# Optimization experiments

Measured on AMD Instinct MI355X. Metric: run time of the kernel, lower is better.

## Reference

```python
import math
import jax, jax.numpy as jnp
import numpy as np

NBINS = 10
MAX_ANGLE = math.pi
KERNEL = 8
POOL_PAD = 1
POOL_STRIDE = 1


def setup_inputs() -> dict:
    key = jax.random.key(0)
    x = jax.random.normal(key, (32, 1, 512, 512), dtype=jnp.float32)
    # Sobel buffer: mat stacked with its transpose -> [2, 1, 3, 3]
    mat = jnp.array([[1.0, 0.0, -1.0], [2.0, 0.0, -2.0], [1.0, 0.0, -1.0]], dtype=jnp.float32)
    weight = jnp.stack([mat, mat.T])[:, None, :, :]
    return {"x": x, "weight": weight}


def reference(x, weight):
    # Sobel gradients: conv2d, stride 1, padding 1 (cross-correlation, same as torch)
    gxy = jax.lax.conv_general_dilated(
        x, weight, window_strides=(1, 1),
        padding=[(1, 1), (1, 1)],
        dimension_numbers=("NCHW", "OIHW", "NCHW"))  # [N,2,H,W]

    norm = jnp.sqrt(gxy[:, 0] ** 2 + gxy[:, 1] ** 2)[:, None]        # [N,1,H,W]
    phase = jnp.arctan2(gxy[:, 0], gxy[:, 1])                        # [N,H,W]
    phase_int = (phase / MAX_ANGLE * NBINS)[:, None]                 # [N,1,H,W]

    # torch `%` is remainder (sign of divisor) == jnp.mod
    b = jnp.floor(phase_int) % NBINS
    t = jnp.ceil(phase_int) % NBINS
    f = phase_int % NBINS
    t_v = norm * (1.0 - (t - f))
    b_v = norm * (1.0 - (f - b))

    idx_b = jnp.floor(phase_int).astype(jnp.int32) % NBINS           # [N,1,H,W]
    idx_t = jnp.ceil(phase_int).astype(jnp.int32) % NBINS

    # scatter into nbins channels: out starts at zero, scatter_ (set) then
    # scatter_add_ -> equivalent to sum of the two one-hot contributions
    bins = jnp.arange(NBINS, dtype=jnp.int32)[None, :, None, None]   # [1,nbins,1,1]
    out = jnp.where(bins == idx_b, b_v, 0.0) + jnp.where(bins == idx_t, t_v, 0.0)  # [N,nbins,H,W]

    # AvgPool2d(kernel=8, stride=1, padding=1, count_include_pad=True)
    summed = jax.lax.reduce_window(
        out, 0.0, jax.lax.add,
        window_dimensions=(1, 1, KERNEL, KERNEL),
        window_strides=(1, 1, POOL_STRIDE, POOL_STRIDE),
        padding=[(0, 0), (0, 0), (POOL_PAD, POOL_PAD), (POOL_PAD, POOL_PAD)])
    return summed / float(KERNEL * KERNEL)
```

## Files before the change

kernel.cpp:

```cpp
#include <hip/hip_runtime.h>
#include <math.h>

#define NB 10
#define H 512
#define W 512
#define HW (H * W)
#define OH 507
#define OW 507
#define TW 32
#define TH 16
#define HC 39
#define HCP 40
#define HR 23
#define IC 41
#define IR 25
#define BD 512
#define BSTRIDE (HR * HCP)
#define HISTF (NB * BSTRIDE)
#define GX 16
#define GY 32
#define NIMG 32
#define NWG (GX * GY * NIMG)

__device__ __forceinline__ float f32mod10(float a) {
    float r = fmodf(a, 10.0f);
    if (r < 0.0f) r = __fadd_rn(r, 10.0f);
    return r;
}

__global__ __launch_bounds__(BD, 8)
void hog_fused(const float* __restrict__ x, float* __restrict__ out) {
    __shared__ __align__(16) float hist[HISTF];
    __shared__ __align__(16) float xin[IR * IC];

    const int orig = blockIdx.x;
    const int swz  = (orig & 7) * (NWG / 8) + (orig >> 3);
    const int tx   = swz & (GX - 1);
    const int ty   = (swz >> 4) & (GY - 1);
    const int n    = swz >> 9;

    const int tid = threadIdx.x;
    const int ox0 = tx * TW;
    const int oy0 = ty * TH;
    const float* __restrict__ xp = x + (size_t)n * HW;

    const int i1 = tid, i2 = tid + BD;
    int r1 = i1 / IC, c1 = i1 - r1 * IC;
    int r2 = i2 / IC, c2 = i2 - r2 * IC;
    int gy1 = oy0 - 2 + r1, gx1 = ox0 - 2 + c1;
    int gy2 = oy0 - 2 + r2, gx2 = ox0 - 2 + c2;
    const bool v1 = (unsigned)gy1 < H && (unsigned)gx1 < W;
    const bool v2 = (unsigned)gy2 < H && (unsigned)gx2 < W;
    float pv1 = v1 ? xp[gy1 * W + gx1] : 0.0f;
    float pv2 = v2 ? xp[gy2 * W + gx2] : 0.0f;
    float pv3 = 0.0f;
    if (tid == 0 && (unsigned)(oy0 + 22) < H && (unsigned)(ox0 + 38) < W)
        pv3 = xp[(oy0 + 22) * W + (ox0 + 38)];

    {
        float4* h4 = (float4*)hist;
        for (int i = tid; i < HISTF / 4; i += BD)
            h4[i] = make_float4(0.f, 0.f, 0.f, 0.f);
    }
    xin[i1] = pv1;
    xin[i2] = pv2;
    if (tid == 0) xin[1024] = pv3;
    __syncthreads();

    for (int p = tid; p < HR * HC; p += BD) {
        int hr = p / HC, hc = p - (p / HC) * HC;
        int hy = oy0 - 1 + hr, hx = ox0 - 1 + hc;
        if ((unsigned)hy >= H || (unsigned)hx >= W) continue;
        const float* xr = &xin[hr * IC + hc];
        float a00 = xr[0],      a01 = xr[1],          a02 = xr[2];
        float a10 = xr[IC],                           a12 = xr[IC + 2];
        float a20 = xr[2 * IC], a21 = xr[2 * IC + 1], a22 = xr[2 * IC + 2];

        float gxv = __fadd_rn(a00, -a02);
        gxv = __fadd_rn(gxv, __fmul_rn(2.0f, a10));
        gxv = __fadd_rn(gxv, -__fmul_rn(2.0f, a12));
        gxv = __fadd_rn(gxv, a20);
        gxv = __fadd_rn(gxv, -a22);
        float gyv = __fadd_rn(a00, __fmul_rn(2.0f, a01));
        gyv = __fadd_rn(gyv, a02);
        gyv = __fadd_rn(gyv, -a20);
        gyv = __fadd_rn(gyv, -__fmul_rn(2.0f, a21));
        gyv = __fadd_rn(gyv, -a22);

        float ay_ = fabsf(gxv), ax_ = fabsf(gyv);
        float hi = fmaxf(ax_, ay_), lo = fminf(ax_, ay_);
        if (hi == 0.0f) continue;
        float nrm = __builtin_amdgcn_sqrtf(
            __fadd_rn(__fmul_rn(gxv, gxv), __fmul_rn(gyv, gyv)));

        bool exact = (hi < 1e-30f) || (hi > 1e30f);
        float pint = 0.0f;
        if (!exact) {
            float t  = lo * __builtin_amdgcn_rcpf(hi);
            bool red = t > 0.41421356f;
            float u  = red ? (t - 1.0f) * __builtin_amdgcn_rcpf(t + 1.0f) : t;
            float z  = u * u;
            float pl = ((8.05374449538e-2f * z - 1.38776856032e-1f) * z
                        + 1.99777106478e-1f) * z - 3.33329491539e-1f;
            float a  = fmaf(u * z, pl, u);
            if (red) a += 0.78539816339744831f;
            if (ay_ > ax_) a = 1.57079632679489662f - a;
            if (gyv < 0.0f) a = 3.14159265358979324f - a;
            float ph = (gxv < 0.0f) ? -a : a;
            pint = ph * 3.18309886183790672f;
            if (fabsf(pint - rintf(pint)) < 1e-4f) exact = true;
        }

        float b_v, t_v;
        int ib, it;
        if (exact) {
            float phf = (float)atan2((double)gxv, (double)gyv);
            float pe  = __fmul_rn(__fdiv_rn(phf, (float)3.14159265358979323846), 10.0f);
            float bfv = floorf(pe), tfv = ceilf(pe);
            float fm = f32mod10(pe), bm = f32mod10(bfv), tm = f32mod10(tfv);
            t_v = __fmul_rn(nrm, __fsub_rn(1.0f, __fsub_rn(tm, fm)));
            b_v = __fmul_rn(nrm, __fsub_rn(1.0f, __fsub_rn(fm, bm)));
            ib = (((int)bfv % NB) + NB) % NB;
            it = (((int)tfv % NB) + NB) % NB;
        } else {
            float bfv  = floorf(pint);
            float frac = pint - bfv;
            float fm   = (pint < 0.0f) ? pint + 10.0f : pint;
            b_v = nrm * (1.0f - frac);
            int bi = (int)bfv;
            ib = (bi < 0) ? bi + 10 : bi;
            if (ib == 9) { it = 0;      t_v = nrm * (1.0f + fm); }
            else         { it = ib + 1; t_v = nrm * frac; }
        }
        int cell = hr * HCP + hc;
        if (ib == it) {
            hist[ib * BSTRIDE + cell] = __fadd_rn(b_v, t_v);
        } else {
            hist[ib * BSTRIDE + cell] = b_v;
            hist[it * BSTRIDE + cell] = t_v;
        }
    }
    __syncthreads();

    for (int q = tid; q < NB * (HCP / 4); q += BD) {
        int b = q / 10, c4 = q - (q / 10) * 10;
        float4* col = (float4*)&hist[b * BSTRIDE + c4 * 4];
        float4 s = make_float4(0.f, 0.f, 0.f, 0.f);
        #pragma unroll
        for (int hr = 0; hr < 8; ++hr) {
            float4 v = col[hr * 10];
            s.x += v.x; s.y += v.y; s.z += v.z; s.w += v.w;
        }
        float4 s0 = s;
        #pragma unroll 4
        for (int i = 1; i < TH; ++i) {
            float4 a = col[(i + 7) * 10];
            float4 d = col[(i - 1) * 10];
            s.x += a.x - d.x; s.y += a.y - d.y;
            s.z += a.z - d.z; s.w += a.w - d.w;
            col[(i - 1) * 10] = s;
        }
        col[22 * 10] = s0;
    }
    __syncthreads();

    float* __restrict__ outn = out + (size_t)n * (NB * OH * OW);
    const float4* h4 = (const float4*)hist;
    for (int u = tid; u < NB * TH * 4; u += BD) {
        int b = u >> 6, i = (u >> 2) & 15, g8 = u & 3;
        int rowf4 = b * (BSTRIDE / 4) + (i == 0 ? 22 : i - 1) * 10 + 2 * g8;
        float4 A = h4[rowf4], B = h4[rowf4 + 1], C = h4[rowf4 + 2], D = h4[rowf4 + 3];
        float o0 = ((A.x + A.y) + (A.z + A.w)) + ((B.x + B.y) + (B.z + B.w));
        float o1 = o0 - A.x + C.x;
        float o2 = o1 - A.y + C.y;
        float o3 = o2 - A.z + C.z;
        float o4 = o3 - A.w + C.w;
        float o5 = o4 - B.x + D.x;
        float o6 = o5 - B.y + D.y;
        float o7 = o6 - B.z + D.z;
        int oy = oy0 + i;
        if (oy < OH) {
            int oxg = ox0 + 8 * g8;
            float* po = outn + (size_t)(b * OH + oy) * OW + oxg;
            if (oxg + 7 < OW) {
                po[0] = o0 * (1.0f / 64.0f); po[1] = o1 * (1.0f / 64.0f);
                po[2] = o2 * (1.0f / 64.0f); po[3] = o3 * (1.0f / 64.0f);
                po[4] = o4 * (1.0f / 64.0f); po[5] = o5 * (1.0f / 64.0f);
                po[6] = o6 * (1.0f / 64.0f); po[7] = o7 * (1.0f / 64.0f);
            } else {
                float ov[8] = {o0, o1, o2, o3, o4, o5, o6, o7};
                #pragma unroll
                for (int j = 0; j < 8; ++j)
                    if (oxg + j < OW) po[j] = ov[j] * (1.0f / 64.0f);
            }
        }
    }
}

extern "C" void kernel_launch(void* const* d_in, const int* in_sizes, int n_in,
                              void* d_out, int out_size, void* d_ws, size_t ws_size,
                              hipStream_t stream) {
    const float* x = (const float*)d_in[0];
    float* out = (float*)d_out;
    hog_fused<<<dim3(NWG), dim3(BD), 0, stream>>>(x, out);
}
```

Measured before the change: 151.6 us.

## Make each workgroup loop over four column tiles with double-buffered histograms

Each workgroup now handles four horizontally adjacent 32x16 tiles in a loop instead of one. The next tile's input is prefetched into registers, the previous tile's output is written from one histogram buffer, and the current tile is scattered into the other buffer. This overlaps global loads and stores with compute and amortizes launch and setup costs across tiles. In exchange it doubles the histogram shared memory, lowers the occupancy hint from 8 to 4, and launches four times fewer workgroups, so there is less parallelism to hide latency.

New measurement: 158.0 us. 1.04x slower.

```diff
diff --git a/kernel.cpp b/kernel.cpp
--- a/kernel.cpp
+++ b/kernel.cpp
@@ -15,12 +15,14 @@
 #define IC 41
 #define IR 25
 #define BD 512
+#define KT 4
 #define BSTRIDE (HR * HCP)
 #define HISTF (NB * BSTRIDE)
-#define GX 16
+#define XINF (IR * IC)
+#define GXS 4
 #define GY 32
 #define NIMG 32
-#define NWG (GX * GY * NIMG)
+#define NWG (GXS * GY * NIMG)
 
 __device__ __forceinline__ float f32mod10(float a) {
     float r = fmodf(a, 10.0f);
@@ -28,172 +30,206 @@
     return r;
 }
 
-__global__ __launch_bounds__(BD, 8)
-void hog_fused(const float* __restrict__ x, float* __restrict__ out) {
-    __shared__ __align__(16) float hist[HISTF];
-    __shared__ __align__(16) float xin[IR * IC];
+__global__ __launch_bounds__(BD, 4)
+void hog_pipe(const float* __restrict__ x, float* __restrict__ out) {
+    __shared__ __align__(16) float hist[2][HISTF];
+    __shared__ __align__(16) float xin[XINF];
 
     const int orig = blockIdx.x;
     const int swz  = (orig & 7) * (NWG / 8) + (orig >> 3);
-    const int tx   = swz & (GX - 1);
-    const int ty   = (swz >> 4) & (GY - 1);
-    const int n    = swz >> 9;
+    const int bxs  = swz & (GXS - 1);
+    const int ty   = (swz >> 2) & (GY - 1);
+    const int n    = swz >> 7;
 
     const int tid = threadIdx.x;
-    const int ox0 = tx * TW;
+    const int oxb = bxs * (KT * TW);
     const int oy0 = ty * TH;
     const float* __restrict__ xp = x + (size_t)n * HW;
-
-    const int i1 = tid, i2 = tid + BD;
-    int r1 = i1 / IC, c1 = i1 - r1 * IC;
-    int r2 = i2 / IC, c2 = i2 - r2 * IC;
-    int gy1 = oy0 - 2 + r1, gx1 = ox0 - 2 + c1;
-    int gy2 = oy0 - 2 + r2, gx2 = ox0 - 2 + c2;
-    const bool v1 = (unsigned)gy1 < H && (unsigned)gx1 < W;
-    const bool v2 = (unsigned)gy2 < H && (unsigned)gx2 < W;
-    float pv1 = v1 ? xp[gy1 * W + gx1] : 0.0f;
-    float pv2 = v2 ? xp[gy2 * W + gx2] : 0.0f;
-    float pv3 = 0.0f;
-    if (tid == 0 && (unsigned)(oy0 + 22) < H && (unsigned)(ox0 + 38) < W)
-        pv3 = xp[(oy0 + 22) * W + (ox0 + 38)];
-
+    float* __restrict__ outn = out + (size_t)n * (NB * OH * OW);
+
+    const int i2 = tid + BD;
+    const int r1 = tid / IC, c1 = tid - r1 * IC;
+    const int r2 = i2 / IC,  c2 = i2 - r2 * IC;
+    const int gy1 = oy0 - 2 + r1, gy2 = oy0 - 2 + r2;
+    const int sp2 = tid + BD;
+    const int hr1 = tid / HC, hc1 = tid - hr1 * HC;
+    const int hr2 = sp2 / HC, hc2 = sp2 - hr2 * HC;
+
+    float pv1, pv2, pv3;
     {
-        float4* h4 = (float4*)hist;
-        for (int i = tid; i < HISTF / 4; i += BD)
-            h4[i] = make_float4(0.f, 0.f, 0.f, 0.f);
+        const int gx1 = oxb - 2 + c1, gx2 = oxb - 2 + c2;
+        pv1 = ((unsigned)gy1 < H && (unsigned)gx1 < W) ? xp[gy1 * W + gx1] : 0.0f;
+        pv2 = ((unsigned)gy2 < H && (unsigned)gx2 < W) ? xp[gy2 * W + gx2] : 0.0f;
+        pv3 = 0.0f;
+        if (tid == 0 && (unsigned)(oy0 + 22) < H && (unsigned)(oxb + 38) < W)
+            pv3 = xp[(oy0 + 22) * W + (oxb + 38)];
     }
-    xin[i1] = pv1;
-    xin[i2] = pv2;
+    {
+        const float4 z4 = make_float4(0.f, 0.f, 0.f, 0.f);
+        float4* h0 = (float4*)&hist[0][0];
+        float4* h1 = (float4*)&hist[1][0];
+        for (int i = tid; i < HISTF / 4; i += BD) { h0[i] = z4; h1[i] = z4; }
+    }
+    xin[tid] = pv1; xin[i2] = pv2;
     if (tid == 0) xin[1024] = pv3;
     __syncthreads();
 
-    for (int p = tid; p < HR * HC; p += BD) {
-        int hr = p / HC, hc = p - (p / HC) * HC;
-        int hy = oy0 - 1 + hr, hx = ox0 - 1 + hc;
-        if ((unsigned)hy >= H || (unsigned)hx >= W) continue;
-        const float* xr = &xin[hr * IC + hc];
-        float a00 = xr[0],      a01 = xr[1],          a02 = xr[2];
-        float a10 = xr[IC],                           a12 = xr[IC + 2];
-        float a20 = xr[2 * IC], a21 = xr[2 * IC + 1], a22 = xr[2 * IC + 2];
-
-        float gxv = __fadd_rn(a00, -a02);
-        gxv = __fadd_rn(gxv, __fmul_rn(2.0f, a10));
-        gxv = __fadd_rn(gxv, -__fmul_rn(2.0f, a12));
-        gxv = __fadd_rn(gxv, a20);
-        gxv = __fadd_rn(gxv, -a22);
-        float gyv = __fadd_rn(a00, __fmul_rn(2.0f, a01));
-        gyv = __fadd_rn(gyv, a02);
-        gyv = __fadd_rn(gyv, -a20);
-        gyv = __fadd_rn(gyv, -__fmul_rn(2.0f, a21));
-        gyv = __fadd_rn(gyv, -a22);
-
-        float ay_ = fabsf(gxv), ax_ = fabsf(gyv);
-        float hi = fmaxf(ax_, ay_), lo = fminf(ax_, ay_);
-        if (hi == 0.0f) continue;
-        float nrm = __builtin_amdgcn_sqrtf(
-            __fadd_rn(__fmul_rn(gxv, gxv), __fmul_rn(gyv, gyv)));
-
-        bool exact = (hi < 1e-30f) || (hi > 1e30f);
-        float pint = 0.0f;
-        if (!exact) {
-            float t  = lo * __builtin_amdgcn_rcpf(hi);
-            bool red = t > 0.41421356f;
-            float u  = red ? (t - 1.0f) * __builtin_amdgcn_rcpf(t + 1.0f) : t;
-            float z  = u * u;
-            float pl = ((8.05374449538e-2f * z - 1.38776856032e-1f) * z
-                        + 1.99777106478e-1f) * z - 3.33329491539e-1f;
-            float a  = fmaf(u * z, pl, u);
-            if (red) a += 0.78539816339744831f;
-            if (ay_ > ax_) a = 1.57079632679489662f - a;
-            if (gyv < 0.0f) a = 3.14159265358979324f - a;
-            float ph = (gxv < 0.0f) ? -a : a;
-            pint = ph * 3.18309886183790672f;
-            if (fabsf(pint - rintf(pint)) < 1e-4f) exact = true;
-        }
-
-        float b_v, t_v;
-        int ib, it;
-        if (exact) {
-            float phf = (float)atan2((double)gxv, (double)gyv);
-            float pe  = __fmul_rn(__fdiv_rn(phf, (float)3.14159265358979323846), 10.0f);
-            float bfv = floorf(pe), tfv = ceilf(pe);
-            float fm = f32mod10(pe), bm = f32mod10(bfv), tm = f32mod10(tfv);
-            t_v = __fmul_rn(nrm, __fsub_rn(1.0f, __fsub_rn(tm, fm)));
-            b_v = __fmul_rn(nrm, __fsub_rn(1.0f, __fsub_rn(fm, bm)));
-            ib = (((int)bfv % NB) + NB) % NB;
-            it = (((int)tfv % NB) + NB) % NB;
-        } else {
-            float bfv  = floorf(pint);
-            float frac = pint - bfv;
-            float fm   = (pint < 0.0f) ? pint + 10.0f : pint;
-            b_v = nrm * (1.0f - frac);
-            int bi = (int)bfv;
-            ib = (bi < 0) ? bi + 10 : bi;
-            if (ib == 9) { it = 0;      t_v = nrm * (1.0f + fm); }
-            else         { it = ib + 1; t_v = nrm * frac; }
-        }
-        int cell = hr * HCP + hc;
-        if (ib == it) {
-            hist[ib * BSTRIDE + cell] = __fadd_rn(b_v, t_v);
-        } else {
-            hist[ib * BSTRIDE + cell] = b_v;
-            hist[it * BSTRIDE + cell] = t_v;
-        }
-    }
-    __syncthreads();
-
-    for (int q = tid; q < NB * (HCP / 4); q += BD) {
-        int b = q / 10, c4 = q - (q / 10) * 10;
-        float4* col = (float4*)&hist[b * BSTRIDE + c4 * 4];
-        float4 s = make_float4(0.f, 0.f, 0.f, 0.f);
-        #pragma unroll
-        for (int hr = 0; hr < 8; ++hr) {
-            float4 v = col[hr * 10];
-            s.x += v.x; s.y += v.y; s.z += v.z; s.w += v.w;
-        }
-        float4 s0 = s;
-        #pragma unroll 4
-        for (int i = 1; i < TH; ++i) {
-            float4 a = col[(i + 7) * 10];
-            float4 d = col[(i - 1) * 10];
-            s.x += a.x - d.x; s.y += a.y - d.y;
-            s.z += a.z - d.z; s.w += a.w - d.w;
-            col[(i - 1) * 10] = s;
-        }
-        col[22 * 10] = s0;
-    }
-    __syncthreads();
-
-    float* __restrict__ outn = out + (size_t)n * (NB * OH * OW);
-    const float4* h4 = (const float4*)hist;
-    for (int u = tid; u < NB * TH * 4; u += BD) {
-        int b = u >> 6, i = (u >> 2) & 15, g8 = u & 3;
-        int rowf4 = b * (BSTRIDE / 4) + (i == 0 ? 22 : i - 1) * 10 + 2 * g8;
-        float4 A = h4[rowf4], B = h4[rowf4 + 1], C = h4[rowf4 + 2], D = h4[rowf4 + 3];
-        float o0 = ((A.x + A.y) + (A.z + A.w)) + ((B.x + B.y) + (B.z + B.w));
-        float o1 = o0 - A.x + C.x;
-        float o2 = o1 - A.y + C.y;
-        float o3 = o2 - A.z + C.z;
-        float o4 = o3 - A.w + C.w;
-        float o5 = o4 - B.x + D.x;
-        float o6 = o5 - B.y + D.y;
-        float o7 = o6 - B.z + D.z;
-        int oy = oy0 + i;
-        if (oy < OH) {
-            int oxg = ox0 + 8 * g8;
-            float* po = outn + (size_t)(b * OH + oy) * OW + oxg;
-            if (oxg + 7 < OW) {
-                po[0] = o0 * (1.0f / 64.0f); po[1] = o1 * (1.0f / 64.0f);
-                po[2] = o2 * (1.0f / 64.0f); po[3] = o3 * (1.0f / 64.0f);
-                po[4] = o4 * (1.0f / 64.0f); po[5] = o5 * (1.0f / 64.0f);
-                po[6] = o6 * (1.0f / 64.0f); po[7] = o7 * (1.0f / 64.0f);
-            } else {
-                float ov[8] = {o0, o1, o2, o3, o4, o5, o6, o7};
-                #pragma unroll
-                for (int j = 0; j < 8; ++j)
-                    if (oxg + j < OW) po[j] = ov[j] * (1.0f / 64.0f);
+    for (int k = 0; k <= KT; ++k) {
+        const int cur = k & 1, prv = cur ^ 1;
+
+        if (k + 1 < KT) {
+            const int ox0n = oxb + (k + 1) * TW;
+            const int gx1 = ox0n - 2 + c1, gx2 = ox0n - 2 + c2;
+            pv1 = ((unsigned)gy1 < H && (unsigned)gx1 < W) ? xp[gy1 * W + gx1] : 0.0f;
+            pv2 = ((unsigned)gy2 < H && (unsigned)gx2 < W) ? xp[gy2 * W + gx2] : 0.0f;
+            pv3 = 0.0f;
+            if (tid == 0 && (unsigned)(oy0 + 22) < H && (unsigned)(ox0n + 38) < W)
+                pv3 = xp[(oy0 + 22) * W + (ox0n + 38)];
+        }
+        if (k > 0) {
+            const int ox0p = oxb + (k - 1) * TW;
+            const float4* h4 = (const float4*)&hist[prv][0];
+            for (int u = tid; u < NB * TH * 4; u += BD) {
+                const int b = u >> 6, i = (u >> 2) & 15, g8 = u & 3;
+                const int rowf4 = b * (BSTRIDE / 4)
+                                + (i == 0 ? 22 : i - 1) * (HCP / 4) + 2 * g8;
+                float4 A = h4[rowf4],     Bv = h4[rowf4 + 1];
+                float4 C = h4[rowf4 + 2], D  = h4[rowf4 + 3];
+                float o0 = ((A.x + A.y) + (A.z + A.w)) + ((Bv.x + Bv.y) + (Bv.z + Bv.w));
+                float o1 = o0 - A.x + C.x;
+                float o2 = o1 - A.y + C.y;
+                float o3 = o2 - A.z + C.z;
+                float o4 = o3 - A.w + C.w;
+                float o5 = o4 - Bv.x + D.x;
+                float o6 = o5 - Bv.y + D.y;
+                float o7 = o6 - Bv.z + D.z;
+                const int oy = oy0 + i;
+                if (oy < OH) {
+                    const int oxg = ox0p + 8 * g8;
+                    float* po = outn + (size_t)(b * OH + oy) * OW + oxg;
+                    if (oxg + 7 < OW) {
+                        po[0] = o0 * (1.0f / 64.0f); po[1] = o1 * (1.0f / 64.0f);
+                        po[2] = o2 * (1.0f / 64.0f); po[3] = o3 * (1.0f / 64.0f);
+                        po[4] = o4 * (1.0f / 64.0f); po[5] = o5 * (1.0f / 64.0f);
+                        po[6] = o6 * (1.0f / 64.0f); po[7] = o7 * (1.0f / 64.0f);
+                    } else {
+                        float ov[8] = {o0, o1, o2, o3, o4, o5, o6, o7};
+                        #pragma unroll
+                        for (int j = 0; j < 8; ++j)
+                            if (oxg + j < OW) po[j] = ov[j] * (1.0f / 64.0f);
+                    }
+                }
             }
         }
+        if (k < KT) {
+            const int ox0 = oxb + k * TW;
+            float* hcur = &hist[cur][0];
+            auto scatter = [&](int hr, int hc) {
+                const int hy = oy0 - 1 + hr, hx = ox0 - 1 + hc;
+                if ((unsigned)hy >= H || (unsigned)hx >= W) return;
+                const float* xr = &xin[hr * IC + hc];
+                float a00 = xr[0],      a01 = xr[1],          a02 = xr[2];
+                float a10 = xr[IC],                           a12 = xr[IC + 2];
+                float a20 = xr[2 * IC], a21 = xr[2 * IC + 1], a22 = xr[2 * IC + 2];
+                float gxv = __fadd_rn(a00, -a02);
+                gxv = __fadd_rn(gxv, __fmul_rn(2.0f, a10));
+                gxv = __fadd_rn(gxv, -__fmul_rn(2.0f, a12));
+                gxv = __fadd_rn(gxv, a20);
+                gxv = __fadd_rn(gxv, -a22);
+                float gyv = __fadd_rn(a00, __fmul_rn(2.0f, a01));
+                gyv = __fadd_rn(gyv, a02);
+                gyv = __fadd_rn(gyv, -a20);
+                gyv = __fadd_rn(gyv, -__fmul_rn(2.0f, a21));
+                gyv = __fadd_rn(gyv, -a22);
+
+                float ay_ = fabsf(gxv), ax_ = fabsf(gyv);
+                float hi = fmaxf(ax_, ay_), lo = fminf(ax_, ay_);
+                if (hi == 0.0f) return;
+                float nrm = __builtin_amdgcn_sqrtf(
+                    __fadd_rn(__fmul_rn(gxv, gxv), __fmul_rn(gyv, gyv)));
+
+                bool exact = (hi < 1e-30f) || (hi > 1e30f);
+                float pint = 0.0f;
+                if (!exact) {
+                    float t  = lo * __builtin_amdgcn_rcpf(hi);
+                    bool red = t > 0.41421356f;
+                    float u  = red ? (t - 1.0f) * __builtin_amdgcn_rcpf(t + 1.0f) : t;
+                    float z  = u * u;
+                    float pl = ((8.05374449538e-2f * z - 1.38776856032e-1f) * z
+                                + 1.99777106478e-1f) * z - 3.33329491539e-1f;
+                    float a  = fmaf(u * z, pl, u);
+                    if (red) a += 0.78539816339744831f;
+                    if (ay_ > ax_) a = 1.57079632679489662f - a;
+                    if (gyv < 0.0f) a = 3.14159265358979324f - a;
+                    float ph = (gxv < 0.0f) ? -a : a;
+                    pint = ph * 3.18309886183790672f;
+                    if (fabsf(pint - rintf(pint)) < 1e-4f) exact = true;
+                }
+
+                float b_v, t_v;
+                int ib, it;
+                if (exact) {
+                    float phf = (float)atan2((double)gxv, (double)gyv);
+                    float pe  = __fmul_rn(__fdiv_rn(phf, (float)3.14159265358979323846), 10.0f);
+                    float bfv = floorf(pe), tfv = ceilf(pe);
+                    float fm = f32mod10(pe), bm = f32mod10(bfv), tm = f32mod10(tfv);
+                    t_v = __fmul_rn(nrm, __fsub_rn(1.0f, __fsub_rn(tm, fm)));
+                    b_v = __fmul_rn(nrm, __fsub_rn(1.0f, __fsub_rn(fm, bm)));
+                    ib = (((int)bfv % NB) + NB) % NB;
+                    it = (((int)tfv % NB) + NB) % NB;
+                } else {
+                    float bfv  = floorf(pint);
+                    float frac = pint - bfv;
+                    float fm   = (pint < 0.0f) ? pint + 10.0f : pint;
+                    b_v = nrm * (1.0f - frac);
+                    int bi = (int)bfv;
+                    ib = (bi < 0) ? bi + 10 : bi;
+                    if (ib == 9) { it = 0;      t_v = nrm * (1.0f + fm); }
+                    else         { it = ib + 1; t_v = nrm * frac; }
+                }
+                const int cell = hr * HCP + hc;
+                if (ib == it) {
+                    hcur[ib * BSTRIDE + cell] = __fadd_rn(b_v, t_v);
+                } else {
+                    hcur[ib * BSTRIDE + cell] = b_v;
+                    hcur[it * BSTRIDE + cell] = t_v;
+                }
+            };
+            scatter(hr1, hc1);
+            if (sp2 < HR * HC) scatter(hr2, hc2);
+        }
+        __syncthreads();
+
+        if (k < KT && tid < NB * (HCP / 4)) {
+            const int b = tid / (HCP / 4), c4 = tid - b * (HCP / 4);
+            float4* col = (float4*)&hist[cur][b * BSTRIDE + c4 * 4];
+            float4 s = make_float4(0.f, 0.f, 0.f, 0.f);
+            #pragma unroll
+            for (int hr = 0; hr < 8; ++hr) {
+                float4 v = col[hr * 10];
+                s.x += v.x; s.y += v.y; s.z += v.z; s.w += v.w;
+            }
+            float4 s0 = s;
+            #pragma unroll 4
+            for (int i = 1; i < TH; ++i) {
+                float4 a = col[(i + 7) * 10];
+                float4 d = col[(i - 1) * 10];
+                s.x += a.x - d.x; s.y += a.y - d.y;
+                s.z += a.z - d.z; s.w += a.w - d.w;
+                col[(i - 1) * 10] = s;
+            }
+            col[22 * 10] = s0;
+        }
+        if (k > 0 && k + 1 < KT) {
+            const float4 z4 = make_float4(0.f, 0.f, 0.f, 0.f);
+            float4* hz = (float4*)&hist[prv][0];
+            for (int i = tid; i < HISTF / 4; i += BD) hz[i] = z4;
+        }
+        if (k + 1 < KT) {
+            xin[tid] = pv1; xin[i2] = pv2;
+            if (tid == 0) xin[1024] = pv3;
+        }
+        if (k < KT) __syncthreads();
     }
 }
 
@@ -202,5 +238,5 @@
                               hipStream_t stream) {
     const float* x = (const float*)d_in[0];
     float* out = (float*)d_out;
-    hog_fused<<<dim3(NWG), dim3(BD), 0, stream>>>(x, out);
+    hog_pipe<<<dim3(NWG), dim3(BD), 0, stream>>>(x, out);
 }
```
